# Kernel optimization log

Measured on AMD Instinct MI355X. Metric: run time of the kernel, lower is better.

The kernel has to match this reference:

```python
import jax, jax.numpy as jnp
import numpy as np
import math

N_HEAD = 8
N_FEAT = 512
D_K = N_FEAT // N_HEAD
B, T = 4, 2048


def setup_inputs() -> dict:
    key = jax.random.key(0)
    ks = jax.random.split(key, 16)
    s = 1.0 / math.sqrt(N_FEAT)
    return {
        "x": jax.random.normal(ks[0], (B, T, N_FEAT), dtype=jnp.float32),
        "pos_emb": jax.random.normal(ks[1], (1, T, N_FEAT), dtype=jnp.float32),
        "Wq": jax.random.normal(ks[2], (N_FEAT, N_FEAT), dtype=jnp.float32) * s,
        "bq": jnp.zeros((N_FEAT,), dtype=jnp.float32),
        "Wk": jax.random.normal(ks[3], (N_FEAT, N_FEAT), dtype=jnp.float32) * s,
        "bk": jnp.zeros((N_FEAT,), dtype=jnp.float32),
        "Wv": jax.random.normal(ks[4], (N_FEAT, N_FEAT), dtype=jnp.float32) * s,
        "bv": jnp.zeros((N_FEAT,), dtype=jnp.float32),
        "Wpos": jax.random.normal(ks[5], (N_FEAT, N_FEAT), dtype=jnp.float32) * s,
        "Wout": jax.random.normal(ks[6], (N_FEAT, N_FEAT), dtype=jnp.float32) * s,
        "bout": jnp.zeros((N_FEAT,), dtype=jnp.float32),
        "pos_bias_u": jax.random.normal(ks[7], (N_HEAD, D_K), dtype=jnp.float32) * 0.05,
        "pos_bias_v": jax.random.normal(ks[8], (N_HEAD, D_K), dtype=jnp.float32) * 0.05,
    }


def reference(x, pos_emb, Wq, bq, Wk, bk, Wv, bv, Wpos, Wout, bout,
              pos_bias_u, pos_bias_v):
    b, t, f = x.shape
    h, d = N_HEAD, D_K
    # QKV projections (torch Linear: y = x @ W.T + b), split into heads -> (B,H,T,d)
    q = (jnp.einsum('btf,of->bto', x, Wq) + bq).reshape(b, t, h, d).transpose(0, 2, 1, 3)
    k = (jnp.einsum('btf,of->bto', x, Wk) + bk).reshape(b, t, h, d).transpose(0, 2, 1, 3)
    v = (jnp.einsum('btf,of->bto', x, Wv) + bv).reshape(b, t, h, d).transpose(0, 2, 1, 3)
    # positional projection: (1, T_pos, F) -> (H, T_pos, d)
    tp = pos_emb.shape[1]
    p = jnp.einsum('ptf,of->pto', pos_emb, Wpos).reshape(tp, h, d).transpose(1, 0, 2)
    q_u = q + pos_bias_u[None, :, None, :]  # (B,H,T,d)
    q_v = q + pos_bias_v[None, :, None, :]
    matrix_ac = jnp.einsum('bhtd,bhsd->bhts', q_u, k)   # content-content
    matrix_bd = jnp.einsum('bhtd,hsd->bhts', q_v, p)    # content-position
    scores = (matrix_ac + matrix_bd) / math.sqrt(d)
    attn = jax.nn.softmax(scores, axis=-1)  # dropout is identity in eval mode
    out = jnp.einsum('bhts,bhsd->bhtd', attn, v)
    out = out.transpose(0, 2, 1, 3).reshape(b, t, h * d)
    return jnp.einsum('btf,of->bto', out, Wout) + bout
```

## Files before the change

### kernel.cpp

```cpp
#include <hip/hip_runtime.h>

typedef float f4 __attribute__((ext_vector_type(4)));
typedef __attribute__((ext_vector_type(8))) short bf16x8;
typedef __attribute__((ext_vector_type(4))) float f32x4;
typedef __attribute__((ext_vector_type(2))) int i32x2;

#define T_SEQ 2048
#define NFEAT 512
#define NHEAD 8
#define DK    64
#define BATCH 4

using gptr_t = const __attribute__((address_space(1))) void*;
using lptr_t = __attribute__((address_space(3))) void*;

#define LOG2E_8 0.18033688011f

static __device__ __forceinline__ short f2bf(float f) {
    unsigned u = __builtin_bit_cast(unsigned, f);
    u += 0x7fff + ((u >> 16) & 1);
    return (short)(u >> 16);
}
static __device__ __forceinline__ float b2f(short s) {
    unsigned u = ((unsigned)(unsigned short)s) << 16;
    return __builtin_bit_cast(float, u);
}
static __device__ __forceinline__ int pkbf(float a, float b) {
    unsigned ua = __builtin_bit_cast(unsigned, a) + 0x8000u;
    unsigned ub = __builtin_bit_cast(unsigned, b) + 0x8000u;
    return (int)((ua >> 16) | (ub & 0xFFFF0000u));
}

__global__ __launch_bounds__(256) void cvt_kernel(
    const float* __restrict__ x, const float* __restrict__ pos,
    const float* __restrict__ Wq, const float* __restrict__ Wk, const float* __restrict__ Wv,
    const float* __restrict__ Wpos, const float* __restrict__ Wout,
    const float* __restrict__ bq, const float* __restrict__ bk, const float* __restrict__ bv,
    short* __restrict__ xb, short* __restrict__ posb, short* __restrict__ wqkv,
    short* __restrict__ wpb, short* __restrict__ wob, float* __restrict__ bqkv)
{
    const int blk = blockIdx.x;
    const float* src; short* dst; int off;
    if      (blk < 2048) { src = x;    dst = xb;          off = blk * 2048; }
    else if (blk < 2560) { src = pos;  dst = posb;        off = (blk - 2048) * 2048; }
    else if (blk < 2688) { src = Wq;   dst = wqkv;        off = (blk - 2560) * 2048; }
    else if (blk < 2816) { src = Wk;   dst = wqkv + 262144; off = (blk - 2688) * 2048; }
    else if (blk < 2944) { src = Wv;   dst = wqkv + 524288; off = (blk - 2816) * 2048; }
    else if (blk < 3072) { src = Wpos; dst = wpb;         off = (blk - 2944) * 2048; }
    else if (blk < 3200) { src = Wout; dst = wob;         off = (blk - 3072) * 2048; }
    else {
        int t = threadIdx.x;
        bqkv[t]        = bq[t];        bqkv[256 + t]  = bq[256 + t];
        bqkv[512 + t]  = bk[t];        bqkv[768 + t]  = bk[256 + t];
        bqkv[1024 + t] = bv[t];        bqkv[1280 + t] = bv[256 + t];
        return;
    }
    int i = off + threadIdx.x * 8;
    f4 a = *(const f4*)(src + i);
    f4 b = *(const f4*)(src + i + 4);
    bf16x8 o;
#pragma unroll
    for (int j = 0; j < 4; ++j) { o[j] = f2bf(a[j]); o[4 + j] = f2bf(b[j]); }
    *(bf16x8*)(dst + i) = o;
}

template<int OUT_BF16>
static __device__ __forceinline__ void gemm_tile(
    short* As, short* Bs,
    const short* __restrict__ A, const short* __restrict__ B,
    const float* __restrict__ bias, void* __restrict__ Cv,
    int N, int K, int row0, int col0)
{
    const int tid = threadIdx.x, lane = tid & 63, wave = tid >> 6;
    const int col = lane & 15, quad = lane >> 4;
    const int wm = (wave >> 1) * 64, wn = (wave & 1) * 64;
    const int rl = lane & 15;

    const short* Abase = A + (size_t)(row0 + wave * 32 + rl) * K + (lane >> 4) * 8;
    const short* Bbase = B + (size_t)(col0 + wave * 32 + rl) * K + (lane >> 4) * 8;

    f32x4 acc[4][4];
#pragma unroll
    for (int i = 0; i < 4; ++i)
#pragma unroll
        for (int j = 0; j < 4; ++j) acc[i][j] = (f32x4){0.f, 0.f, 0.f, 0.f};

    for (int k0 = 0; k0 < K; k0 += 64) {
        __syncthreads();
#pragma unroll
        for (int c = 0; c < 2; ++c)
#pragma unroll
            for (int hf = 0; hf < 2; ++hf) {
                __builtin_amdgcn_global_load_lds((gptr_t)(Abase + (size_t)(16 * c) * K + k0 + hf * 32),
                                                 (lptr_t)(As + wave * 2048 + c * 1024 + hf * 512), 16, 0, 0);
                __builtin_amdgcn_global_load_lds((gptr_t)(Bbase + (size_t)(16 * c) * K + k0 + hf * 32),
                                                 (lptr_t)(Bs + wave * 2048 + c * 1024 + hf * 512), 16, 0, 0);
            }
        __syncthreads();
#pragma unroll
        for (int kt = 0; kt < 2; ++kt) {
            bf16x8 af[4], bfr[4];
#pragma unroll
            for (int mt = 0; mt < 4; ++mt)
                af[mt] = *(const bf16x8*)&As[((wm >> 4) + mt) * 1024 + (kt * 4 + quad) * 128 + col * 8];
#pragma unroll
            for (int nt = 0; nt < 4; ++nt)
                bfr[nt] = *(const bf16x8*)&Bs[((wn >> 4) + nt) * 1024 + (kt * 4 + quad) * 128 + col * 8];
#pragma unroll
            for (int mt = 0; mt < 4; ++mt)
#pragma unroll
                for (int nt = 0; nt < 4; ++nt)
                    acc[mt][nt] = __builtin_amdgcn_mfma_f32_16x16x32_bf16(af[mt], bfr[nt], acc[mt][nt], 0, 0, 0);
        }
    }

    float bv4[4];
#pragma unroll
    for (int nt = 0; nt < 4; ++nt)
        bv4[nt] = bias ? bias[col0 + wn + nt * 16 + col] : 0.f;
#pragma unroll
    for (int mt = 0; mt < 4; ++mt)
#pragma unroll
        for (int reg = 0; reg < 4; ++reg) {
            int r = row0 + wm + mt * 16 + quad * 4 + reg;
#pragma unroll
            for (int nt = 0; nt < 4; ++nt) {
                int c = col0 + wn + nt * 16 + col;
                float v = acc[mt][nt][reg] + bv4[nt];
                if (OUT_BF16) ((short*)Cv)[(size_t)r * N + c] = f2bf(v);
                else          ((float*)Cv)[(size_t)r * N + c] = v;
            }
        }
}

__global__ __launch_bounds__(256) void gemm_qkv_pos(
    const short* __restrict__ xb, const short* __restrict__ wqkv,
    const float* __restrict__ bqkv, short* __restrict__ QKV,
    const short* __restrict__ posb, const short* __restrict__ wpb,
    short* __restrict__ Pm)
{
    __shared__ short As[8192], Bs[8192];
    const int bid = blockIdx.x;
    if (bid < 768) {
        const int xcd = bid & 7, s = bid >> 3;
        const int row = xcd * 8 + (s & 7), colt = s >> 3;
        gemm_tile<1>(As, Bs, xb, wqkv, bqkv, QKV, 1536, 512, row * 128, colt * 128);
    } else {
        const int t = bid - 768;
        gemm_tile<1>(As, Bs, posb, wpb, nullptr, Pm, 512, 512, (t / 4) * 128, (t % 4) * 128);
    }
}

__global__ __launch_bounds__(256) void gemm_out_kernel(
    const short* __restrict__ A, const short* __restrict__ B,
    const float* __restrict__ bias, float* __restrict__ C)
{
    __shared__ short As[8192], Bs[8192];
    const int bid = blockIdx.x;
    const int xcd = bid & 7, s = bid >> 3;
    const int row = xcd * 8 + (s & 7), colt = s >> 3;
    gemm_tile<0>(As, Bs, A, B, bias, C, 512, 512, row * 128, colt * 128);
}

__global__ __launch_bounds__(256) void kvprep_kernel(
    const short* __restrict__ qkv, const short* __restrict__ pm,
    const float* __restrict__ u, const float* __restrict__ vb,
    short* __restrict__ kp, short* __restrict__ vt, float* __restrict__ cb)
{
    __shared__ short tile[64][72];
    const int tid = threadIdx.x, lr = tid >> 2, lc = (tid & 3) * 16;
    const int bh = blockIdx.y, b = bh >> 3, h = bh & 7, s0 = blockIdx.x * 64;

    const short* kptr = qkv + (size_t)(b * T_SEQ + s0 + lr) * 1536 + 512 + h * DK + lc;
    const short* pptr = pm + (size_t)(s0 + lr) * NFEAT + h * DK + lc;
    const short* vptr = qkv + (size_t)(b * T_SEQ + s0 + lr) * 1536 + 1024 + h * DK + lc;
    bf16x8 k0_ = *(const bf16x8*)kptr,       k1_ = *(const bf16x8*)(kptr + 8);
    bf16x8 p0_ = *(const bf16x8*)pptr,       p1_ = *(const bf16x8*)(pptr + 8);
    bf16x8 v0_ = *(const bf16x8*)vptr,       v1_ = *(const bf16x8*)(vptr + 8);

    float c = 0.f;
    bf16x8 o0, o1;
#pragma unroll
    for (int j = 0; j < 8; ++j) {
        float kf = b2f(k0_[j]), pf = b2f(p0_[j]);
        o0[j] = f2bf(kf + pf);
        c += u[h * DK + lc + j] * kf + vb[h * DK + lc + j] * pf;
        float kf1 = b2f(k1_[j]), pf1 = b2f(p1_[j]);
        o1[j] = f2bf(kf1 + pf1);
        c += u[h * DK + lc + 8 + j] * kf1 + vb[h * DK + lc + 8 + j] * pf1;
    }
    short* kpd = kp + ((size_t)bh * T_SEQ + s0 + lr) * DK + lc;
    *(bf16x8*)kpd       = o0;
    *(bf16x8*)(kpd + 8) = o1;
    c += __shfl_xor(c, 1);
    c += __shfl_xor(c, 2);
    if ((tid & 3) == 0) cb[(size_t)bh * T_SEQ + s0 + lr] = LOG2E_8 * c;

    *(bf16x8*)&tile[lr][lc]     = v0_;
    *(bf16x8*)&tile[lr][lc + 8] = v1_;
    __syncthreads();
    short* dst = vt + (size_t)(bh * DK + lr) * T_SEQ + s0 + lc;
    bf16x8 t0_, t1_;
#pragma unroll
    for (int j = 0; j < 8; ++j) { t0_[j] = tile[lc + j][lr]; t1_[j] = tile[lc + 8 + j][lr]; }
    *(bf16x8*)dst       = t0_;
    *(bf16x8*)(dst + 8) = t1_;
}

__global__ __launch_bounds__(512, 8) void attn_kernel(
    const short* __restrict__ qkv, const short* __restrict__ kp,
    const short* __restrict__ vt, const float* __restrict__ cb,
    short* __restrict__ attO)
{
    __shared__ __align__(16) short KPs[64][72], Vts[64][72], Ps[8][16][72];
    __shared__ float cs[64];
    const int tid = threadIdx.x, lane = tid & 63, wave = tid >> 6;
    const int col = lane & 15, quad = lane >> 4;
    const int idx = blockIdx.x;
    const int xcd = idx & 7, slot = idx >> 3;
    const int bh = (slot >> 4) * 8 + xcd;
    const int t0 = (slot & 15) * 128;
    const int b = bh >> 3, h = bh & 7;

    const short* qbase = qkv + (size_t)(b * T_SEQ + t0 + wave * 16 + col) * 1536 + h * DK + quad * 8;
    bf16x8 qa0 = *(const bf16x8*)qbase;
    bf16x8 qa1 = *(const bf16x8*)(qbase + 32);

    const int lr8 = tid >> 3, lc8 = (tid & 7) * 8;
    const int rho = 4 * (lr8 & 15) + (lr8 >> 4);

    bf16x8 kpr = *(const bf16x8*)(kp + ((size_t)bh * T_SEQ + rho) * DK + lc8);
    bf16x8 vtr = *(const bf16x8*)(vt + ((size_t)(bh * DK + lr8)) * T_SEQ + lc8);
    float cbr = (tid < 64) ? cb[(size_t)bh * T_SEQ + tid] : 0.f;

    f32x4 Oacc[4];
    float lsum[4] = {0.f, 0.f, 0.f, 0.f};
#pragma unroll
    for (int i = 0; i < 4; ++i) Oacc[i] = (f32x4){0.f, 0.f, 0.f, 0.f};

    for (int s0 = 0; s0 < T_SEQ; s0 += 64) {
        __syncthreads();
        *(bf16x8*)&KPs[lr8][lc8] = kpr;
        *(bf16x8*)&Vts[lr8][lc8] = vtr;
        if (tid < 64) cs[tid] = cbr;
        __syncthreads();

        const int sn = (s0 + 64) & (T_SEQ - 1);
        kpr = *(const bf16x8*)(kp + ((size_t)bh * T_SEQ + sn + rho) * DK + lc8);
        vtr = *(const bf16x8*)(vt + ((size_t)(bh * DK + lr8)) * T_SEQ + sn + lc8);
        if (tid < 64) cbr = cb[(size_t)bh * T_SEQ + sn + tid];

        f32x4 S[4];
#pragma unroll
        for (int nt = 0; nt < 4; ++nt) S[nt] = (f32x4){0.f, 0.f, 0.f, 0.f};
#pragma unroll
        for (int nt = 0; nt < 4; ++nt) {
            bf16x8 b0 = *(const bf16x8*)&KPs[nt * 16 + col][quad * 8];
            S[nt] = __builtin_amdgcn_mfma_f32_16x16x32_bf16(qa0, b0, S[nt], 0, 0, 0);
            bf16x8 b1 = *(const bf16x8*)&KPs[nt * 16 + col][32 + quad * 8];
            S[nt] = __builtin_amdgcn_mfma_f32_16x16x32_bf16(qa1, b1, S[nt], 0, 0, 0);
        }
        const f4 cv = *(const f4*)&cs[4 * col];
#pragma unroll
        for (int reg = 0; reg < 4; ++reg) {
            float e0 = __builtin_amdgcn_exp2f(fmaf(S[0][reg], LOG2E_8, cv[0]));
            float e1 = __builtin_amdgcn_exp2f(fmaf(S[1][reg], LOG2E_8, cv[1]));
            float e2 = __builtin_amdgcn_exp2f(fmaf(S[2][reg], LOG2E_8, cv[2]));
            float e3 = __builtin_amdgcn_exp2f(fmaf(S[3][reg], LOG2E_8, cv[3]));
            lsum[reg] += (e0 + e1) + (e2 + e3);
            i32x2 pw; pw[0] = pkbf(e0, e1); pw[1] = pkbf(e2, e3);
            *(i32x2*)&Ps[wave][quad * 4 + reg][4 * col] = pw;
        }
#pragma unroll
        for (int kt = 0; kt < 2; ++kt) {
            bf16x8 pa = *(const bf16x8*)&Ps[wave][col][kt * 32 + quad * 8];
#pragma unroll
            for (int dt = 0; dt < 4; ++dt) {
                bf16x8 vb = *(const bf16x8*)&Vts[dt * 16 + col][kt * 32 + quad * 8];
                Oacc[dt] = __builtin_amdgcn_mfma_f32_16x16x32_bf16(pa, vb, Oacc[dt], 0, 0, 0);
            }
        }
    }
#pragma unroll
    for (int reg = 0; reg < 4; ++reg) {
        float l = lsum[reg];
#pragma unroll
        for (int off = 1; off < 16; off <<= 1) l += __shfl_xor(l, off);
        float inv = 1.f / l;
        int t = t0 + wave * 16 + quad * 4 + reg;
        short* op = attO + (size_t)(b * T_SEQ + t) * NFEAT + h * DK;
#pragma unroll
        for (int dt = 0; dt < 4; ++dt)
            op[dt * 16 + col] = f2bf(Oacc[dt][reg] * inv);
    }
}

extern "C" void kernel_launch(void* const* d_in, const int* in_sizes, int n_in,
                              void* d_out, int out_size, void* d_ws, size_t ws_size,
                              hipStream_t stream)
{
    const float* x    = (const float*)d_in[0];
    const float* pos  = (const float*)d_in[1];
    const float* Wq   = (const float*)d_in[2];
    const float* bq   = (const float*)d_in[3];
    const float* Wk   = (const float*)d_in[4];
    const float* bk   = (const float*)d_in[5];
    const float* Wv   = (const float*)d_in[6];
    const float* bv   = (const float*)d_in[7];
    const float* Wpos = (const float*)d_in[8];
    const float* Wout = (const float*)d_in[9];
    const float* bout = (const float*)d_in[10];
    const float* pbu  = (const float*)d_in[11];
    const float* pbv  = (const float*)d_in[12];
    float* out = (float*)d_out;

    short* xb   = (short*)d_ws;
    short* posb = xb   + 4194304;
    short* wqkv = posb + 1048576;
    short* wpb  = wqkv + 786432;
    short* wob  = wpb  + 262144;
    short* QKV  = wob  + 262144;
    short* Pm   = QKV  + 12582912;
    short* KP   = Pm   + 1048576;
    short* Vt   = KP   + 4194304;
    short* AttO = Vt   + 4194304;
    float* bqkv = (float*)(AttO + 4194304);
    float* Cb   = bqkv + 1536;

    cvt_kernel<<<dim3(3201), dim3(256), 0, stream>>>(x, pos, Wq, Wk, Wv, Wpos, Wout, bq, bk, bv,
                                                     xb, posb, wqkv, wpb, wob, bqkv);
    gemm_qkv_pos<<<dim3(832), dim3(256), 0, stream>>>(xb, wqkv, bqkv, QKV, posb, wpb, Pm);
    kvprep_kernel<<<dim3(T_SEQ / 64, BATCH * NHEAD), dim3(256), 0, stream>>>(QKV, Pm, pbu, pbv, KP, Vt, Cb);
    attn_kernel<<<dim3(512), dim3(512), 0, stream>>>(QKV, KP, Vt, Cb, AttO);
    gemm_out_kernel<<<dim3(256), dim3(256), 0, stream>>>(AttO, wob, bout, out);
}
```

Baseline: 243.0 us.

## Give each attention wave two 16-row query groups to reuse K/V fragments

The attention kernel now runs 4 waves of 256 threads per block instead of 8 waves, and each wave handles 32 query rows as two 16-row groups. Each K and Vt fragment read from LDS feeds two MFMAs, halving LDS fragment reads per unit of work, and each thread loads twice as much K/V tile data per step. The cost is more accumulator registers per thread and fewer waves per block to hide latency. A redundant first exp2 for e0 is left in but overwritten, so it is probably removed by the compiler.

Measured after the change: 226.9 us. 1.07x faster.

```diff
diff --git a/kernel.cpp b/kernel.cpp
--- a/kernel.cpp
+++ b/kernel.cpp
@@ -207,12 +207,12 @@
     *(bf16x8*)(dst + 8) = t1_;
 }
 
-__global__ __launch_bounds__(512, 8) void attn_kernel(
+__global__ __launch_bounds__(256, 4) void attn_kernel(
     const short* __restrict__ qkv, const short* __restrict__ kp,
     const short* __restrict__ vt, const float* __restrict__ cb,
     short* __restrict__ attO)
 {
-    __shared__ __align__(16) short KPs[64][72], Vts[64][72], Ps[8][16][72];
+    __shared__ __align__(16) short KPs[64][72], Vts[64][72], Ps[4][32][72];
     __shared__ float cs[64];
     const int tid = threadIdx.x, lane = tid & 63, wave = tid >> 6;
     const int col = lane & 15, quad = lane >> 4;
@@ -222,77 +222,104 @@
     const int t0 = (slot & 15) * 128;
     const int b = bh >> 3, h = bh & 7;
 
-    const short* qbase = qkv + (size_t)(b * T_SEQ + t0 + wave * 16 + col) * 1536 + h * DK + quad * 8;
-    bf16x8 qa0 = *(const bf16x8*)qbase;
-    bf16x8 qa1 = *(const bf16x8*)(qbase + 32);
-
-    const int lr8 = tid >> 3, lc8 = (tid & 7) * 8;
-    const int rho = 4 * (lr8 & 15) + (lr8 >> 4);
-
-    bf16x8 kpr = *(const bf16x8*)(kp + ((size_t)bh * T_SEQ + rho) * DK + lc8);
-    bf16x8 vtr = *(const bf16x8*)(vt + ((size_t)(bh * DK + lr8)) * T_SEQ + lc8);
+    bf16x8 qa[2][2];
+#pragma unroll
+    for (int g = 0; g < 2; ++g) {
+        const short* qb = qkv + (size_t)(b * T_SEQ + t0 + wave * 32 + g * 16 + col) * 1536 + h * DK + quad * 8;
+        qa[g][0] = *(const bf16x8*)qb;
+        qa[g][1] = *(const bf16x8*)(qb + 32);
+    }
+
+    const int lr  = tid >> 2;
+    const int lcq = (tid & 3) * 16;
+    const int rho = 4 * (lr & 15) + (lr >> 4);
+
+    const short* kpbase = kp + (size_t)bh * T_SEQ * DK;
+    const short* vtbase = vt + (size_t)bh * DK * T_SEQ;
+
+    bf16x8 kpr0 = *(const bf16x8*)(kpbase + (size_t)rho * DK + lcq);
+    bf16x8 kpr1 = *(const bf16x8*)(kpbase + (size_t)rho * DK + lcq + 8);
+    bf16x8 vtr0 = *(const bf16x8*)(vtbase + (size_t)lr * T_SEQ + lcq);
+    bf16x8 vtr1 = *(const bf16x8*)(vtbase + (size_t)lr * T_SEQ + lcq + 8);
     float cbr = (tid < 64) ? cb[(size_t)bh * T_SEQ + tid] : 0.f;
 
-    f32x4 Oacc[4];
-    float lsum[4] = {0.f, 0.f, 0.f, 0.f};
-#pragma unroll
-    for (int i = 0; i < 4; ++i) Oacc[i] = (f32x4){0.f, 0.f, 0.f, 0.f};
+    f32x4 Oacc[2][4];
+    float lsum[2][4];
+#pragma unroll
+    for (int g = 0; g < 2; ++g)
+#pragma unroll
+        for (int i = 0; i < 4; ++i) { Oacc[g][i] = (f32x4){0.f, 0.f, 0.f, 0.f}; lsum[g][i] = 0.f; }
 
     for (int s0 = 0; s0 < T_SEQ; s0 += 64) {
         __syncthreads();
-        *(bf16x8*)&KPs[lr8][lc8] = kpr;
-        *(bf16x8*)&Vts[lr8][lc8] = vtr;
+        *(bf16x8*)&KPs[lr][lcq]     = kpr0;
+        *(bf16x8*)&KPs[lr][lcq + 8] = kpr1;
+        *(bf16x8*)&Vts[lr][lcq]     = vtr0;
+        *(bf16x8*)&Vts[lr][lcq + 8] = vtr1;
         if (tid < 64) cs[tid] = cbr;
         __syncthreads();
 
         const int sn = (s0 + 64) & (T_SEQ - 1);
-        kpr = *(const bf16x8*)(kp + ((size_t)bh * T_SEQ + sn + rho) * DK + lc8);
-        vtr = *(const bf16x8*)(vt + ((size_t)(bh * DK + lr8)) * T_SEQ + sn + lc8);
+        kpr0 = *(const bf16x8*)(kpbase + (size_t)(sn + rho) * DK + lcq);
+        kpr1 = *(const bf16x8*)(kpbase + (size_t)(sn + rho) * DK + lcq + 8);
+        vtr0 = *(const bf16x8*)(vtbase + (size_t)lr * T_SEQ + sn + lcq);
+        vtr1 = *(const bf16x8*)(vtbase + (size_t)lr * T_SEQ + sn + lcq + 8);
         if (tid < 64) cbr = cb[(size_t)bh * T_SEQ + sn + tid];
 
-        f32x4 S[4];
-#pragma unroll
-        for (int nt = 0; nt < 4; ++nt) S[nt] = (f32x4){0.f, 0.f, 0.f, 0.f};
+        f32x4 S[2][4];
+#pragma unroll
+        for (int g = 0; g < 2; ++g)
+#pragma unroll
+            for (int nt = 0; nt < 4; ++nt) S[g][nt] = (f32x4){0.f, 0.f, 0.f, 0.f};
 #pragma unroll
         for (int nt = 0; nt < 4; ++nt) {
             bf16x8 b0 = *(const bf16x8*)&KPs[nt * 16 + col][quad * 8];
-            S[nt] = __builtin_amdgcn_mfma_f32_16x16x32_bf16(qa0, b0, S[nt], 0, 0, 0);
             bf16x8 b1 = *(const bf16x8*)&KPs[nt * 16 + col][32 + quad * 8];
-            S[nt] = __builtin_amdgcn_mfma_f32_16x16x32_bf16(qa1, b1, S[nt], 0, 0, 0);
+            S[0][nt] = __builtin_amdgcn_mfma_f32_16x16x32_bf16(qa[0][0], b0, S[0][nt], 0, 0, 0);
+            S[1][nt] = __builtin_amdgcn_mfma_f32_16x16x32_bf16(qa[1][0], b0, S[1][nt], 0, 0, 0);
+            S[0][nt] = __builtin_amdgcn_mfma_f32_16x16x32_bf16(qa[0][1], b1, S[0][nt], 0, 0, 0);
+            S[1][nt] = __builtin_amdgcn_mfma_f32_16x16x32_bf16(qa[1][1], b1, S[1][nt], 0, 0, 0);
         }
         const f4 cv = *(const f4*)&cs[4 * col];
 #pragma unroll
-        for (int reg = 0; reg < 4; ++reg) {
-            float e0 = __builtin_amdgcn_exp2f(fmaf(S[0][reg], LOG2E_8, cv[0]));
-            float e1 = __builtin_amdgcn_exp2f(fmaf(S[1][reg], LOG2E_8, cv[1]));
-            float e2 = __builtin_amdgcn_exp2f(fmaf(S[2][reg], LOG2E_8, cv[2]));
-            float e3 = __builtin_amdgcn_exp2f(fmaf(S[3][reg], LOG2E_8, cv[3]));
-            lsum[reg] += (e0 + e1) + (e2 + e3);
-            i32x2 pw; pw[0] = pkbf(e0, e1); pw[1] = pkbf(e2, e3);
-            *(i32x2*)&Ps[wave][quad * 4 + reg][4 * col] = pw;
-        }
+        for (int g = 0; g < 2; ++g)
+#pragma unroll
+            for (int reg = 0; reg < 4; ++reg) {
+                float e0 = __builtin_amdgcn_exp2f(fmaf(S[0 + g * 0][0][reg], LOG2E_8, cv[0]));
+                e0 = __builtin_amdgcn_exp2f(fmaf(S[g][0][reg], LOG2E_8, cv[0]));
+                float e1 = __builtin_amdgcn_exp2f(fmaf(S[g][1][reg], LOG2E_8, cv[1]));
+                float e2 = __builtin_amdgcn_exp2f(fmaf(S[g][2][reg], LOG2E_8, cv[2]));
+                float e3 = __builtin_amdgcn_exp2f(fmaf(S[g][3][reg], LOG2E_8, cv[3]));
+                lsum[g][reg] += (e0 + e1) + (e2 + e3);
+                i32x2 pw; pw[0] = pkbf(e0, e1); pw[1] = pkbf(e2, e3);
+                *(i32x2*)&Ps[wave][g * 16 + quad * 4 + reg][4 * col] = pw;
+            }
 #pragma unroll
         for (int kt = 0; kt < 2; ++kt) {
-            bf16x8 pa = *(const bf16x8*)&Ps[wave][col][kt * 32 + quad * 8];
+            bf16x8 pa0 = *(const bf16x8*)&Ps[wave][col][kt * 32 + quad * 8];
+            bf16x8 pa1 = *(const bf16x8*)&Ps[wave][16 + col][kt * 32 + quad * 8];
 #pragma unroll
             for (int dt = 0; dt < 4; ++dt) {
                 bf16x8 vb = *(const bf16x8*)&Vts[dt * 16 + col][kt * 32 + quad * 8];
-                Oacc[dt] = __builtin_amdgcn_mfma_f32_16x16x32_bf16(pa, vb, Oacc[dt], 0, 0, 0);
+                Oacc[0][dt] = __builtin_amdgcn_mfma_f32_16x16x32_bf16(pa0, vb, Oacc[0][dt], 0, 0, 0);
+                Oacc[1][dt] = __builtin_amdgcn_mfma_f32_16x16x32_bf16(pa1, vb, Oacc[1][dt], 0, 0, 0);
             }
         }
     }
 #pragma unroll
-    for (int reg = 0; reg < 4; ++reg) {
-        float l = lsum[reg];
-#pragma unroll
-        for (int off = 1; off < 16; off <<= 1) l += __shfl_xor(l, off);
-        float inv = 1.f / l;
-        int t = t0 + wave * 16 + quad * 4 + reg;
-        short* op = attO + (size_t)(b * T_SEQ + t) * NFEAT + h * DK;
-#pragma unroll
-        for (int dt = 0; dt < 4; ++dt)
-            op[dt * 16 + col] = f2bf(Oacc[dt][reg] * inv);
-    }
+    for (int g = 0; g < 2; ++g)
+#pragma unroll
+        for (int reg = 0; reg < 4; ++reg) {
+            float l = lsum[g][reg];
+#pragma unroll
+            for (int off = 1; off < 16; off <<= 1) l += __shfl_xor(l, off);
+            float inv = 1.f / l;
+            int t = t0 + wave * 32 + g * 16 + quad * 4 + reg;
+            short* op = attO + (size_t)(b * T_SEQ + t) * NFEAT + h * DK;
+#pragma unroll
+            for (int dt = 0; dt < 4; ++dt)
+                op[dt * 16 + col] = f2bf(Oacc[g][dt][reg] * inv);
+        }
 }
 
 extern "C" void kernel_launch(void* const* d_in, const int* in_sizes, int n_in,
@@ -331,6 +358,6 @@
                                                      xb, posb, wqkv, wpb, wob, bqkv);
     gemm_qkv_pos<<<dim3(832), dim3(256), 0, stream>>>(xb, wqkv, bqkv, QKV, posb, wpb, Pm);
     kvprep_kernel<<<dim3(T_SEQ / 64, BATCH * NHEAD), dim3(256), 0, stream>>>(QKV, Pm, pbu, pbv, KP, Vt, Cb);
-    attn_kernel<<<dim3(512), dim3(512), 0, stream>>>(QKV, KP, Vt, Cb, AttO);
+    attn_kernel<<<dim3(512), dim3(256), 0, stream>>>(QKV, KP, Vt, Cb, AttO);
     gemm_out_kernel<<<dim3(256), dim3(256), 0, stream>>>(AttO, wob, bout, out);
 }
```
